# Performance work log

Hardware: AMD Instinct MI355X
Metric: run time of the kernel (lower is better)

## Reference

```python
import jax, jax.numpy as jnp
import numpy as np

B, C, T, H, W = 2, 512, 4, 32, 32
NH = 8          # num_heads
GROUPS = 32     # GroupNorm groups
EPS = 1e-5      # GroupNorm eps (torch default)


def setup_inputs() -> dict:
    key = jax.random.key(0)
    k0, k1, k2 = jax.random.split(key, 3)
    s = 0.02
    return {
        "x": jax.random.normal(k0, (B, C, T, H, W), jnp.float32),
        "gn_w": jnp.ones((C,), jnp.float32),
        "gn_b": jnp.zeros((C,), jnp.float32),
        "qkv_w": jax.random.normal(k1, (3 * C, C), jnp.float32) * s,
        "qkv_b": jnp.zeros((3 * C,), jnp.float32),
        "out_w": jax.random.normal(k2, (C, C), jnp.float32) * s,
        "out_b": jnp.zeros((C,), jnp.float32),
    }


def reference(x, gn_w, gn_b, qkv_w, qkv_b, out_w, out_b):
    Bb, Cc, Tt, Hh, Ww = x.shape
    N = Tt * Hh * Ww
    hd = Cc // NH

    # GroupNorm(32, C): normalize over (C//G, T, H, W) per group, biased var
    xg = x.reshape(Bb, GROUPS, -1)
    mean = jnp.mean(xg, axis=-1, keepdims=True)
    var = jnp.var(xg, axis=-1, keepdims=True)
    h = ((xg - mean) * jax.lax.rsqrt(var + EPS)).reshape(Bb, Cc, N)
    h = h * gn_w[None, :, None] + gn_b[None, :, None]

    # 1x1 Conv3d qkv == per-token linear over channels
    qkv = jnp.einsum('oc,bcn->bon', qkv_w, h) + qkv_b[None, :, None]
    qkv = qkv.reshape(Bb, 3, NH, hd, N).transpose(1, 0, 2, 4, 3)  # [3,B,nh,N,hd]
    q, k, v = qkv[0], qkv[1], qkv[2]

    scale = 1.0 / np.sqrt(hd).astype(np.float32)
    attn = jax.nn.softmax(jnp.einsum('bhnd,bhmd->bhnm', q, k) * scale, axis=-1)
    o = jnp.einsum('bhnm,bhmd->bhnd', attn, v)  # [B,nh,N,hd]

    # Faithful to original: h.permute(1,2,0,3).reshape(B,C,T,H,W)
    o = o.transpose(1, 2, 0, 3).reshape(Bb, Cc, N)
    o = jnp.einsum('oc,bcn->bon', out_w, o) + out_b[None, :, None]
    return x + o.reshape(Bb, Cc, Tt, Hh, Ww)
```

## Files before the change

kernel.cpp:

```cpp
#include <hip/hip_runtime.h>
#include <stdint.h>

#define B_    2
#define C_    512
#define NH_   8
#define HD_   64
#define N_    4096
#define G_    32
#define K_    512
#define EPS_  1e-5f
#define QSCALE_ 0.18033688011112042f

typedef __bf16 bf16;
typedef __attribute__((ext_vector_type(8))) __bf16 bf16x8;
typedef __attribute__((ext_vector_type(4))) float f32x4;

__global__ __launch_bounds__(256) void prep_k(const float* __restrict__ qkv_w,
                                              const float* __restrict__ out_w,
                                              const float* __restrict__ x,
                                              bf16* __restrict__ qkvwb,
                                              bf16* __restrict__ outwb,
                                              float* __restrict__ part) {
  const int blk = blockIdx.x;
  const int t = threadIdx.x;
  if (blk < 1024) {
    const int i = blk * 256 + t;
    const int n0 = (3 * C_ * C_) / 4;
    const float* s = (i < n0) ? qkv_w : out_w;
    bf16* d = (i < n0) ? qkvwb : outwb;
    const int k = (i < n0) ? i : i - n0;
    f32x4 v = *reinterpret_cast<const f32x4*>(s + (size_t)k * 4);
    bf16 o[4] = {(bf16)v[0], (bf16)v[1], (bf16)v[2], (bf16)v[3]};
    *reinterpret_cast<uint64_t*>(d + (size_t)k * 4) = *reinterpret_cast<uint64_t*>(o);
  } else {
    const int bb = blk - 1024;
    const float* p = x + (size_t)bb * 16384;
    float s1 = 0.f, s2 = 0.f;
    for (int i = 0; i < 16; ++i) {
      f32x4 v = *reinterpret_cast<const f32x4*>(p + (size_t)(i * 256 + t) * 4);
#pragma unroll
      for (int j = 0; j < 4; ++j) { float f = v[j]; s1 += f; s2 += f * f; }
    }
#pragma unroll
    for (int o = 32; o > 0; o >>= 1) { s1 += __shfl_down(s1, o); s2 += __shfl_down(s2, o); }
    __shared__ float a1[4], a2[4];
    if ((t & 63) == 0) { a1[t >> 6] = s1; a2[t >> 6] = s2; }
    __syncthreads();
    if (t == 0) {
      part[bb * 2]     = a1[0] + a1[1] + a1[2] + a1[3];
      part[bb * 2 + 1] = a2[0] + a2[1] + a2[2] + a2[3];
    }
  }
}

__global__ __launch_bounds__(256) void gn_apply_k(const float* __restrict__ x,
                                                  const float* __restrict__ part,
                                                  const float* __restrict__ gw,
                                                  const float* __restrict__ gb,
                                                  bf16* __restrict__ hT) {
  __shared__ float tile[64][65];
  const int n0 = blockIdx.x * 64, c0 = blockIdx.y * 64, b = blockIdx.z;
  const int t = threadIdx.x;
  {
    const int cc = t >> 2;
    const int nn = (t & 3) * 16;
    const int c = c0 + cc;
    const int bg = b * G_ + (c >> 4);
    float s1 = 0.f, s2 = 0.f;
#pragma unroll
    for (int q = 0; q < 4; ++q) {
      s1 += part[(bg * 4 + q) * 2];
      s2 += part[(bg * 4 + q) * 2 + 1];
    }
    const float mean = s1 * (1.f / 65536.f);
    const float var  = s2 * (1.f / 65536.f) - mean * mean;
    const float rstd = rsqrtf(var + EPS_);
    const float sw = gw[c] * rstd;
    const float sb = gb[c] - mean * sw;
    const float* xp = x + ((size_t)(b * C_ + c)) * N_ + n0 + nn;
#pragma unroll
    for (int q = 0; q < 4; ++q) {
      f32x4 v = *reinterpret_cast<const f32x4*>(xp + q * 4);
#pragma unroll
      for (int j = 0; j < 4; ++j) tile[cc][nn + q * 4 + j] = v[j] * sw + sb;
    }
  }
  __syncthreads();
  {
    const int rn = t >> 2;
    const int ch = (t & 3) * 16;
    bf16* hp = hT + ((size_t)b * N_ + n0 + rn) * C_ + c0 + ch;
    bf16x8 o0, o1;
#pragma unroll
    for (int j = 0; j < 8; ++j) {
      o0[j] = (bf16)tile[ch + j][rn];
      o1[j] = (bf16)tile[ch + 8 + j][rn];
    }
    *reinterpret_cast<bf16x8*>(hp)     = o0;
    *reinterpret_cast<bf16x8*>(hp + 8) = o1;
  }
}

template <int EPI>
__global__ __launch_bounds__(256) void gemm_bt_k(const bf16* __restrict__ A,
                                                 const bf16* __restrict__ BT,
                                                 const float* __restrict__ bias,
                                                 bf16* __restrict__ out0,
                                                 bf16* __restrict__ out1,
                                                 bf16* __restrict__ out2,
                                                 float* __restrict__ outf,
                                                 const float* __restrict__ xres) {
  __shared__ __align__(16) bf16 As[128][72];
  __shared__ __align__(16) bf16 Bs[128][72];
  const int t = threadIdx.x;
  const int w = t >> 6, lane = t & 63;
  const int quad = lane >> 4, l15 = lane & 15;
  const int m0 = blockIdx.y * 128, n0 = blockIdx.x * 128, b = blockIdx.z;
  const bf16* Ab = A + (size_t)m0 * K_;
  const bf16* Bb = BT + ((size_t)b * N_ + n0) * K_;
  const int srow = t >> 1;
  const int sk = (t & 1) * 32;

  f32x4 acc[4][4] = {};

  for (int kc = 0; kc < K_ / 64; ++kc) {
    __syncthreads();
    {
      const bf16* ag = Ab + (size_t)srow * K_ + kc * 64 + sk;
      const bf16* bg = Bb + (size_t)srow * K_ + kc * 64 + sk;
#pragma unroll
      for (int c = 0; c < 4; ++c) {
        *reinterpret_cast<bf16x8*>(&As[srow][sk + c * 8]) = *reinterpret_cast<const bf16x8*>(ag + c * 8);
        *reinterpret_cast<bf16x8*>(&Bs[srow][sk + c * 8]) = *reinterpret_cast<const bf16x8*>(bg + c * 8);
      }
    }
    __syncthreads();
    bf16x8 af[4][2], bfv[4][2];
#pragma unroll
    for (int i = 0; i < 4; ++i) {
      af[i][0] = *reinterpret_cast<const bf16x8*>(&As[(w >> 1) * 64 + i * 16 + l15][quad * 8]);
      af[i][1] = *reinterpret_cast<const bf16x8*>(&As[(w >> 1) * 64 + i * 16 + l15][quad * 8 + 32]);
    }
#pragma unroll
    for (int j = 0; j < 4; ++j) {
      bfv[j][0] = *reinterpret_cast<const bf16x8*>(&Bs[(w & 1) * 64 + j * 16 + l15][quad * 8]);
      bfv[j][1] = *reinterpret_cast<const bf16x8*>(&Bs[(w & 1) * 64 + j * 16 + l15][quad * 8 + 32]);
    }
#pragma unroll
    for (int i = 0; i < 4; ++i)
#pragma unroll
      for (int j = 0; j < 4; ++j) {
        acc[i][j] = __builtin_amdgcn_mfma_f32_16x16x32_bf16(af[i][0], bfv[j][0], acc[i][j], 0, 0, 0);
        acc[i][j] = __builtin_amdgcn_mfma_f32_16x16x32_bf16(af[i][1], bfv[j][1], acc[i][j], 0, 0, 0);
      }
  }

  const int rowbase = m0 + (w >> 1) * 64;
  const int colbase = n0 + (w & 1) * 64;
  if (EPI == 0) {
    const int which = m0 >> 9;
    if (which < 2) {
      bf16* dst = (which == 0) ? out0 : out1;
      const float sc = (which == 0) ? (float)QSCALE_ : 1.0f;
#pragma unroll
      for (int i = 0; i < 4; ++i) {
        const int mbase = rowbase + i * 16 + quad * 4;
        const int head = (mbase >> 6) & 7, d0 = mbase & 63;
        float bi[4];
#pragma unroll
        for (int r = 0; r < 4; ++r) bi[r] = bias[mbase + r];
#pragma unroll
        for (int j = 0; j < 4; ++j) {
          const int n = colbase + j * 16 + l15;
          union { bf16 h[4]; uint64_t u; } pk;
#pragma unroll
          for (int r = 0; r < 4; ++r) pk.h[r] = (bf16)((acc[i][j][r] + bi[r]) * sc);
          *reinterpret_cast<uint64_t*>(dst + ((size_t)(b * NH_ + head) * N_ + n) * HD_ + d0) = pk.u;
        }
      }
    } else {
#pragma unroll
      for (int i = 0; i < 4; ++i) {
        const int mbase = rowbase + i * 16 + quad * 4;
        const int head = (mbase >> 6) & 7;
#pragma unroll
        for (int r = 0; r < 4; ++r) {
          const int d = (mbase + r) & 63;
          const float bi = bias[mbase + r];
#pragma unroll
          for (int j = 0; j < 4; ++j) {
            const int n = colbase + j * 16 + l15;
            out2[((size_t)(b * NH_ + head) * HD_ + d) * N_ + n] = (bf16)(acc[i][j][r] + bi);
          }
        }
      }
    }
  } else {
#pragma unroll
    for (int i = 0; i < 4; ++i) {
#pragma unroll
      for (int r = 0; r < 4; ++r) {
        const int m = rowbase + i * 16 + quad * 4 + r;
        const float bi = bias[m];
#pragma unroll
        for (int j = 0; j < 4; ++j) {
          const int n = colbase + j * 16 + l15;
          const size_t idx = ((size_t)(b * C_ + m)) * N_ + n;
          outf[idx] = acc[i][j][r] + bi + xres[idx];
        }
      }
    }
  }
}

__global__ __launch_bounds__(256, 2) void attn_k(const bf16* __restrict__ qb,
                                                 const bf16* __restrict__ kb,
                                                 const bf16* __restrict__ vb,
                                                 bf16* __restrict__ oT) {
  __shared__ __align__(16) char smem[55296];
  bf16* Ps = (bf16*)(smem + 36864);
  bf16* Ot = (bf16*)smem;

  const int t = threadIdx.x;
  const int w = t >> 6, lane = t & 63, quad = lane >> 4, l15 = lane & 15;
  const int rblk = blockIdx.x;
  const int bh = blockIdx.y, head = bh & 7, b = bh >> 3;
  const bf16* qh = qb + (size_t)bh * N_ * HD_;
  const bf16* kh = kb + (size_t)bh * N_ * HD_;
  const bf16* vh = vb + (size_t)bh * HD_ * N_;

  bf16x8 qa[2][2];
#pragma unroll
  for (int b2 = 0; b2 < 2; ++b2) {
    const int bd = w + 4 * b2;
    const bf16* qp = qh + ((size_t)((bd * 16 + l15) * 32 + rblk)) * HD_ + quad * 8;
    qa[b2][0] = *reinterpret_cast<const bf16x8*>(qp);
    qa[b2][1] = *reinterpret_cast<const bf16x8*>(qp + 32);
  }

  f32x4 acc[2][4] = {};
  float lsum[2][4] = {};

  const int sr = t >> 3, sc = (t & 7) * 8;
  const int s0 = (sr & 3) * 16 + (sr >> 2);
  const int s1 = ((sr + 32) & 3) * 16 + ((sr + 32) >> 2);

  {
    *reinterpret_cast<bf16x8*>((bf16*)smem + s0 * 72 + sc) =
        *reinterpret_cast<const bf16x8*>(kh + (size_t)sr * HD_ + sc);
    *reinterpret_cast<bf16x8*>((bf16*)smem + s1 * 72 + sc) =
        *reinterpret_cast<const bf16x8*>(kh + (size_t)(sr + 32) * HD_ + sc);
    bf16* Vb0 = (bf16*)(smem + 9216);
    *reinterpret_cast<bf16x8*>(Vb0 + sr * 72 + sc) =
        *reinterpret_cast<const bf16x8*>(vh + (size_t)sr * N_ + sc);
    *reinterpret_cast<bf16x8*>(Vb0 + (sr + 32) * 72 + sc) =
        *reinterpret_cast<const bf16x8*>(vh + (size_t)(sr + 32) * N_ + sc);
  }
  __syncthreads();

  for (int kt = 0; kt < 64; ++kt) {
    bf16* curK = (bf16*)(smem + (kt & 1) * 18432);
    bf16* curV = (bf16*)(smem + (kt & 1) * 18432 + 9216);

    bf16x8 kr0, kr1, vr0, vr1;
    if (kt != 63) {
      const bf16* kg = kh + ((size_t)(kt + 1) * 64) * HD_;
      kr0 = *reinterpret_cast<const bf16x8*>(kg + (size_t)sr * HD_ + sc);
      kr1 = *reinterpret_cast<const bf16x8*>(kg + (size_t)(sr + 32) * HD_ + sc);
      const bf16* vg = vh + (size_t)(kt + 1) * 64;
      vr0 = *reinterpret_cast<const bf16x8*>(vg + (size_t)sr * N_ + sc);
      vr1 = *reinterpret_cast<const bf16x8*>(vg + (size_t)(sr + 32) * N_ + sc);
    }

    bf16x8 kf0[4], kf1[4];
#pragma unroll
    for (int mt = 0; mt < 4; ++mt) {
      kf0[mt] = *reinterpret_cast<const bf16x8*>(curK + (mt * 16 + l15) * 72 + quad * 8);
      kf1[mt] = *reinterpret_cast<const bf16x8*>(curK + (mt * 16 + l15) * 72 + quad * 8 + 32);
    }

#pragma unroll
    for (int b2 = 0; b2 < 2; ++b2) {
      f32x4 S[4];
#pragma unroll
      for (int mt = 0; mt < 4; ++mt) {
        f32x4 zz = {0.f, 0.f, 0.f, 0.f};
        zz = __builtin_amdgcn_mfma_f32_16x16x32_bf16(qa[b2][0], kf0[mt], zz, 0, 0, 0);
        S[mt] = __builtin_amdgcn_mfma_f32_16x16x32_bf16(qa[b2][1], kf1[mt], zz, 0, 0, 0);
      }
      bf16* Pw = Ps + ((w << 1) | b2) * 1152;
#pragma unroll
      for (int r = 0; r < 4; ++r) {
        float p0 = __builtin_amdgcn_exp2f(S[0][r]);
        float p1 = __builtin_amdgcn_exp2f(S[1][r]);
        float p2 = __builtin_amdgcn_exp2f(S[2][r]);
        float p3 = __builtin_amdgcn_exp2f(S[3][r]);
        lsum[b2][r] += (p0 + p1) + (p2 + p3);
        union { bf16 h[4]; uint64_t u; } pk;
        pk.h[0] = (bf16)p0; pk.h[1] = (bf16)p1; pk.h[2] = (bf16)p2; pk.h[3] = (bf16)p3;
        *reinterpret_cast<uint64_t*>(Pw + (quad * 4 + r) * 72 + l15 * 4) = pk.u;
      }
    }
    asm volatile("s_waitcnt lgkmcnt(0)" ::: "memory");
    bf16x8 pa[2][2];
#pragma unroll
    for (int b2 = 0; b2 < 2; ++b2) {
      bf16* Pw = Ps + ((w << 1) | b2) * 1152;
      pa[b2][0] = *reinterpret_cast<const bf16x8*>(Pw + l15 * 72 + quad * 8);
      pa[b2][1] = *reinterpret_cast<const bf16x8*>(Pw + l15 * 72 + quad * 8 + 32);
    }
#pragma unroll
    for (int dt = 0; dt < 4; ++dt) {
      bf16x8 vf0 = *reinterpret_cast<const bf16x8*>(curV + (dt * 16 + l15) * 72 + quad * 8);
      bf16x8 vf1 = *reinterpret_cast<const bf16x8*>(curV + (dt * 16 + l15) * 72 + quad * 8 + 32);
      acc[0][dt] = __builtin_amdgcn_mfma_f32_16x16x32_bf16(pa[0][0], vf0, acc[0][dt], 0, 0, 0);
      acc[0][dt] = __builtin_amdgcn_mfma_f32_16x16x32_bf16(pa[0][1], vf1, acc[0][dt], 0, 0, 0);
      acc[1][dt] = __builtin_amdgcn_mfma_f32_16x16x32_bf16(pa[1][0], vf0, acc[1][dt], 0, 0, 0);
      acc[1][dt] = __builtin_amdgcn_mfma_f32_16x16x32_bf16(pa[1][1], vf1, acc[1][dt], 0, 0, 0);
    }

    if (kt != 63) {
      bf16* nK = (bf16*)(smem + ((kt + 1) & 1) * 18432);
      bf16* nV = (bf16*)(smem + ((kt + 1) & 1) * 18432 + 9216);
      *reinterpret_cast<bf16x8*>(nK + s0 * 72 + sc) = kr0;
      *reinterpret_cast<bf16x8*>(nK + s1 * 72 + sc) = kr1;
      *reinterpret_cast<bf16x8*>(nV + sr * 72 + sc) = vr0;
      *reinterpret_cast<bf16x8*>(nV + (sr + 32) * 72 + sc) = vr1;
    }
    __syncthreads();
  }

  float inv[2][4];
#pragma unroll
  for (int b2 = 0; b2 < 2; ++b2)
#pragma unroll
    for (int r = 0; r < 4; ++r) {
      float l = lsum[b2][r];
#pragma unroll
      for (int o = 1; o < 16; o <<= 1) l += __shfl_xor(l, o);
      inv[b2][r] = 1.f / l;
    }

#pragma unroll
  for (int b2 = 0; b2 < 2; ++b2) {
    const int bd = w + 4 * b2;
#pragma unroll
    for (int dt = 0; dt < 4; ++dt) {
      union { bf16 h[4]; uint64_t u; } o4;
#pragma unroll
      for (int r = 0; r < 4; ++r) o4.h[r] = (bf16)(acc[b2][dt][r] * inv[b2][r]);
      *reinterpret_cast<uint64_t*>(Ot + (dt * 16 + l15) * 136 + bd * 16 + quad * 4) = o4.u;
    }
  }
  __syncthreads();
  {
    const int d = t >> 2, ic = (t & 3) * 32;
    bf16* op = oT + (size_t)(head >> 2) * N_ * C_ +
               ((size_t)(rblk * 128 + b * 64 + d)) * C_ + (head & 3) * 128 + ic;
#pragma unroll
    for (int c = 0; c < 4; ++c)
      *reinterpret_cast<bf16x8*>(op + c * 8) =
          *reinterpret_cast<const bf16x8*>(Ot + d * 136 + ic + c * 8);
  }
}

extern "C" void kernel_launch(void* const* d_in, const int* in_sizes, int n_in,
                              void* d_out, int out_size, void* d_ws, size_t ws_size,
                              hipStream_t stream) {
  const float* x     = (const float*)d_in[0];
  const float* gn_w  = (const float*)d_in[1];
  const float* gn_b  = (const float*)d_in[2];
  const float* qkv_w = (const float*)d_in[3];
  const float* qkv_b = (const float*)d_in[4];
  const float* out_w = (const float*)d_in[5];
  const float* out_b = (const float*)d_in[6];
  float* out = (float*)d_out;

  char* ws = (char*)d_ws;
  const size_t SZ = (size_t)B_ * C_ * N_ * sizeof(bf16);
  float* part  = (float*)ws;
  bf16* hT    = (bf16*)(ws + 4096);
  bf16* qbuf  = (bf16*)(ws + 4096 + SZ);
  bf16* kbuf  = (bf16*)(ws + 4096 + 2 * SZ);
  bf16* vbuf  = (bf16*)(ws + 4096 + 3 * SZ);
  bf16* oT    = (bf16*)(ws + 4096 + 4 * SZ);
  bf16* qkvwb = (bf16*)(ws + 4096 + 5 * SZ);
  bf16* outwb = qkvwb + (size_t)3 * C_ * C_;

  prep_k<<<dim3(1280), dim3(256), 0, stream>>>(qkv_w, out_w, x, qkvwb, outwb, part);
  gn_apply_k<<<dim3(N_ / 64, C_ / 64, B_), dim3(256), 0, stream>>>(x, part, gn_w, gn_b, hT);
  gemm_bt_k<0><<<dim3(N_ / 128, (3 * C_) / 128, B_), dim3(256), 0, stream>>>(
      qkvwb, hT, qkv_b, qbuf, kbuf, vbuf, nullptr, nullptr);
  attn_k<<<dim3(32, B_ * NH_), dim3(256), 0, stream>>>(qbuf, kbuf, vbuf, oT);
  gemm_bt_k<1><<<dim3(N_ / 128, C_ / 128, B_), dim3(256), 0, stream>>>(
      outwb, oT, out_b, nullptr, nullptr, nullptr, out, x);
}
```

Baseline: 215.8 us.

## Share one P staging tile per warp and raise attention occupancy to three blocks

The attention kernel now computes both row-blocks' score tiles first and preloads the V fragments into registers. It then stages P for each row-block through a single per-warp LDS tile, used one after the other, instead of two separate tiles. This cuts shared memory per block from 55296 to 46080 bytes and raises the launch bound to three blocks per CU, aiming at higher occupancy and better latency hiding. The cost is more live registers (both S tiles plus all V fragments), which risks spills under the tighter register budget. With only 512 blocks in the grid, the extra occupancy may add little.

```diff
diff --git a/kernel.cpp b/kernel.cpp
--- a/kernel.cpp
+++ b/kernel.cpp
@@ -213,11 +213,11 @@
   }
 }
 
-__global__ __launch_bounds__(256, 2) void attn_k(const bf16* __restrict__ qb,
+__global__ __launch_bounds__(256, 3) void attn_k(const bf16* __restrict__ qb,
                                                  const bf16* __restrict__ kb,
                                                  const bf16* __restrict__ vb,
                                                  bf16* __restrict__ oT) {
-  __shared__ __align__(16) char smem[55296];
+  __shared__ __align__(16) char smem[46080];
   bf16* Ps = (bf16*)(smem + 36864);
   bf16* Ot = (bf16*)smem;
 
@@ -244,6 +244,7 @@
   const int sr = t >> 3, sc = (t & 7) * 8;
   const int s0 = (sr & 3) * 16 + (sr >> 2);
   const int s1 = ((sr + 32) & 3) * 16 + ((sr + 32) >> 2);
+  bf16* Pw = Ps + w * 1152;
 
   {
     *reinterpret_cast<bf16x8*>((bf16*)smem + s0 * 72 + sc) =
@@ -278,45 +279,44 @@
       kf0[mt] = *reinterpret_cast<const bf16x8*>(curK + (mt * 16 + l15) * 72 + quad * 8);
       kf1[mt] = *reinterpret_cast<const bf16x8*>(curK + (mt * 16 + l15) * 72 + quad * 8 + 32);
     }
-
-#pragma unroll
-    for (int b2 = 0; b2 < 2; ++b2) {
-      f32x4 S[4];
+    f32x4 S[2][4];
+#pragma unroll
+    for (int b2 = 0; b2 < 2; ++b2)
 #pragma unroll
       for (int mt = 0; mt < 4; ++mt) {
         f32x4 zz = {0.f, 0.f, 0.f, 0.f};
         zz = __builtin_amdgcn_mfma_f32_16x16x32_bf16(qa[b2][0], kf0[mt], zz, 0, 0, 0);
-        S[mt] = __builtin_amdgcn_mfma_f32_16x16x32_bf16(qa[b2][1], kf1[mt], zz, 0, 0, 0);
-      }
-      bf16* Pw = Ps + ((w << 1) | b2) * 1152;
+        S[b2][mt] = __builtin_amdgcn_mfma_f32_16x16x32_bf16(qa[b2][1], kf1[mt], zz, 0, 0, 0);
+      }
+
+    bf16x8 vf0[4], vf1[4];
+#pragma unroll
+    for (int dt = 0; dt < 4; ++dt) {
+      vf0[dt] = *reinterpret_cast<const bf16x8*>(curV + (dt * 16 + l15) * 72 + quad * 8);
+      vf1[dt] = *reinterpret_cast<const bf16x8*>(curV + (dt * 16 + l15) * 72 + quad * 8 + 32);
+    }
+
+#pragma unroll
+    for (int b2 = 0; b2 < 2; ++b2) {
 #pragma unroll
       for (int r = 0; r < 4; ++r) {
-        float p0 = __builtin_amdgcn_exp2f(S[0][r]);
-        float p1 = __builtin_amdgcn_exp2f(S[1][r]);
-        float p2 = __builtin_amdgcn_exp2f(S[2][r]);
-        float p3 = __builtin_amdgcn_exp2f(S[3][r]);
+        float p0 = __builtin_amdgcn_exp2f(S[b2][0][r]);
+        float p1 = __builtin_amdgcn_exp2f(S[b2][1][r]);
+        float p2 = __builtin_amdgcn_exp2f(S[b2][2][r]);
+        float p3 = __builtin_amdgcn_exp2f(S[b2][3][r]);
         lsum[b2][r] += (p0 + p1) + (p2 + p3);
         union { bf16 h[4]; uint64_t u; } pk;
         pk.h[0] = (bf16)p0; pk.h[1] = (bf16)p1; pk.h[2] = (bf16)p2; pk.h[3] = (bf16)p3;
         *reinterpret_cast<uint64_t*>(Pw + (quad * 4 + r) * 72 + l15 * 4) = pk.u;
       }
-    }
-    asm volatile("s_waitcnt lgkmcnt(0)" ::: "memory");
-    bf16x8 pa[2][2];
-#pragma unroll
-    for (int b2 = 0; b2 < 2; ++b2) {
-      bf16* Pw = Ps + ((w << 1) | b2) * 1152;
-      pa[b2][0] = *reinterpret_cast<const bf16x8*>(Pw + l15 * 72 + quad * 8);
-      pa[b2][1] = *reinterpret_cast<const bf16x8*>(Pw + l15 * 72 + quad * 8 + 32);
-    }
-#pragma unroll
-    for (int dt = 0; dt < 4; ++dt) {
-      bf16x8 vf0 = *reinterpret_cast<const bf16x8*>(curV + (dt * 16 + l15) * 72 + quad * 8);
-      bf16x8 vf1 = *reinterpret_cast<const bf16x8*>(curV + (dt * 16 + l15) * 72 + quad * 8 + 32);
-      acc[0][dt] = __builtin_amdgcn_mfma_f32_16x16x32_bf16(pa[0][0], vf0, acc[0][dt], 0, 0, 0);
-      acc[0][dt] = __builtin_amdgcn_mfma_f32_16x16x32_bf16(pa[0][1], vf1, acc[0][dt], 0, 0, 0);
-      acc[1][dt] = __builtin_amdgcn_mfma_f32_16x16x32_bf16(pa[1][0], vf0, acc[1][dt], 0, 0, 0);
-      acc[1][dt] = __builtin_amdgcn_mfma_f32_16x16x32_bf16(pa[1][1], vf1, acc[1][dt], 0, 0, 0);
+      asm volatile("s_waitcnt lgkmcnt(0)" ::: "memory");
+      bf16x8 pa0 = *reinterpret_cast<const bf16x8*>(Pw + l15 * 72 + quad * 8);
+      bf16x8 pa1 = *reinterpret_cast<const bf16x8*>(Pw + l15 * 72 + quad * 8 + 32);
+#pragma unroll
+      for (int dt = 0; dt < 4; ++dt) {
+        acc[b2][dt] = __builtin_amdgcn_mfma_f32_16x16x32_bf16(pa0, vf0[dt], acc[b2][dt], 0, 0, 0);
+        acc[b2][dt] = __builtin_amdgcn_mfma_f32_16x16x32_bf16(pa1, vf1[dt], acc[b2][dt], 0, 0, 0);
+      }
     }
 
     if (kt != 63) {
```

Result: no change. 215.6 us (-0.1%).
